# Optimization experiments

Measured on AMD Instinct MI355X. Metric: run time of the kernel, lower is better.

Reference implementation:

```python
import jax, jax.numpy as jnp
import numpy as np

B, T, H, E = 8, 2048, 512, 512

def setup_inputs() -> dict:
    key = jax.random.key(0)
    k1, k2, k3, k4 = jax.random.split(key, 4)
    tokens = jax.random.normal(k1, (B, T, H), dtype=jnp.float32)
    # Linear(hidden,embed,bias=False): stored as (in,out) so Q = tokens @ Wq
    Wq = jax.random.normal(k2, (H, E), dtype=jnp.float32) / np.sqrt(H)
    Wk = jax.random.normal(k3, (H, E), dtype=jnp.float32) / np.sqrt(H)
    Wv = jax.random.normal(k4, (H, H), dtype=jnp.float32) / np.sqrt(H)
    return {"tokens": tokens, "Wq": Wq, "Wk": Wk, "Wv": Wv}

def reference(tokens, Wq, Wk, Wv):
    Q = jnp.einsum('bth,he->bte', tokens, Wq)   # [B,T,E]
    K = jnp.einsum('bsh,he->bse', tokens, Wk)   # [B,T,E]
    V = jnp.einsum('bsh,hd->bsd', tokens, Wv)   # [B,T,H]
    scoremats = jnp.einsum('bte,bse->bts', Q, K)  # [B,T,T]
    # NOTE: softmax over axis=1 (query axis t), matching F.softmax(dim=1)
    attnmats = jax.nn.softmax(scoremats, axis=1)
    ctx_vecs = jnp.einsum('bts,bsh->bth', attnmats, V)  # [B,T,H]
    return ctx_vecs
```

## Files before the change

### kernel.cpp

```cpp
#include <hip/hip_runtime.h>

typedef _Float16 f16;
typedef _Float16 f16x8 __attribute__((ext_vector_type(8)));
typedef _Float16 f16x4 __attribute__((ext_vector_type(4)));
typedef float   f32x4 __attribute__((ext_vector_type(4)));

#define LOG2E 1.44269504088896340736f

__device__ __forceinline__ f32x4 mfma_f16(f16x8 a, f16x8 b, f32x4 c){
  return __builtin_amdgcn_mfma_f32_16x16x32_f16(a, b, c, 0, 0, 0);
}
__device__ __forceinline__ float fexp2(float x){ return __builtin_amdgcn_exp2f(x); }

__device__ __forceinline__ void gld16(void* lds, const void* g){
  __builtin_amdgcn_global_load_lds(
      (const __attribute__((address_space(1))) unsigned int*)g,
      (__attribute__((address_space(3))) unsigned int*)lds,
      16, 0, 0);
}


__global__ __launch_bounds__(256) void k_prep_g(const float* __restrict__ Wq,
                                                const float* __restrict__ Wk,
                                                f16* __restrict__ B16){
  __shared__ float ak[32][36];
  __shared__ float aq[32][36];
  const int n0 = blockIdx.y * 32, e0 = blockIdx.x * 32;
  const int u = threadIdx.x;
  const int ty = u >> 4, tx = u & 15;
  float acc[2][2] = {};
  for (int x0 = 0; x0 < 512; x0 += 32){
    __syncthreads();
    {
      int r = u >> 3, c4 = (u & 7) * 4;
      *(float4*)&ak[r][c4] = *(const float4*)&Wk[(n0 + r) * 512 + x0 + c4];
      *(float4*)&aq[r][c4] = *(const float4*)&Wq[(e0 + r) * 512 + x0 + c4];
    }
    __syncthreads();
#pragma unroll 8
    for (int x = 0; x < 32; ++x){
      float k0 = ak[ty * 2 + 0][x], k1 = ak[ty * 2 + 1][x];
      float q0 = aq[tx * 2 + 0][x], q1 = aq[tx * 2 + 1][x];
      acc[0][0] += k0 * q0; acc[0][1] += k0 * q1;
      acc[1][0] += k1 * q0; acc[1][1] += k1 * q1;
    }
  }
#pragma unroll
  for (int i = 0; i < 2; ++i)
#pragma unroll
    for (int j = 0; j < 2; ++j)
      B16[(size_t)(n0 + ty * 2 + i) * 512 + e0 + tx * 2 + j] = (f16)acc[i][j];
}

__global__ __launch_bounds__(256) void k_prep_wv(const float* __restrict__ Wv,
                                                 f16* __restrict__ B16){
  __shared__ float t[64][72];
  const int e0 = blockIdx.x * 64, h0 = blockIdx.y * 64;
  const int u = threadIdx.x;
#pragma unroll
  for (int k = 0; k < 4; ++k){
    int idx = u + k * 256; int r = idx >> 4, c4 = (idx & 15) * 4;
    *(float4*)&t[r][c4] = *(const float4*)&Wv[(e0 + r) * 512 + h0 + c4];
  }
  __syncthreads();
#pragma unroll
  for (int k = 0; k < 4; ++k){
    int idx = u + k * 256; int j = idx >> 4, i4 = (idx & 15) * 4;
#pragma unroll
    for (int c = 0; c < 4; ++c)
      B16[(size_t)(512 + h0 + j) * 512 + e0 + i4 + c] = (f16)t[i4 + c][j];
  }
}

__global__ __launch_bounds__(256) void k_cast(const float* __restrict__ tok,
                                              f16* __restrict__ T16){
  int i = blockIdx.x * 256 + threadIdx.x;
  const float4* p = (const float4*)tok + (size_t)i * 2;
  float4 a = p[0], b = p[1];
  f16x8 h;
  h[0] = (f16)a.x; h[1] = (f16)a.y; h[2] = (f16)a.z; h[3] = (f16)a.w;
  h[4] = (f16)b.x; h[5] = (f16)b.y; h[6] = (f16)b.z; h[7] = (f16)b.w;
  *((f16x8*)T16 + i) = h;
}

__global__ __launch_bounds__(256, 4) void k_gemm(const f16* __restrict__ T16,
                                                 const f16* __restrict__ B16,
                                                 f16* __restrict__ QG,
                                                 f16* __restrict__ VT){
  __shared__ __align__(16) f16 Abuf[128 * 64];
  __shared__ __align__(16) f16 Bbuf[128 * 64];
  const int tb = blockIdx.x, nb = blockIdx.y;
  const int u = threadIdx.x;
  const int w = u >> 6, l = u & 63, lr = l & 15, lq = l >> 4;
  const int sx8 = (l & 7) ^ (l >> 3), hi8 = l >> 3;
  const int wm = (w & 1) * 64, wn = (w >> 1) * 64;
  f32x4 acc[4][4] = {};
  const f16* sa0 = T16 + (size_t)tb * 128 * 512;
  const f16* sb0 = B16 + (size_t)nb * 128 * 512;
  for (int c = 0; c < 8; ++c){
    {
      const f16* sa = sa0 + c * 64;
      const f16* sb_ = sb0 + c * 64;
#pragma unroll
      for (int k = 0; k < 4; ++k){
        int i = w * 4 + k;
        int row = i * 8 + hi8;
        gld16((char*)Abuf + i * 1024, sa  + (size_t)row * 512 + sx8 * 8);
        gld16((char*)Bbuf + i * 1024, sb_ + (size_t)row * 512 + sx8 * 8);
      }
    }
    __syncthreads();
#pragma unroll
    for (int es = 0; es < 2; ++es){
      f16x8 af[4], bf[4];
#pragma unroll
      for (int mt = 0; mt < 4; ++mt){
        int row = wm + mt * 16 + lr;
        af[mt] = *(const f16x8*)((const char*)Abuf + row * 128 + (((es * 4 + lq) ^ (row & 7)) << 4));
      }
#pragma unroll
      for (int nt = 0; nt < 4; ++nt){
        int row = wn + nt * 16 + lr;
        bf[nt] = *(const f16x8*)((const char*)Bbuf + row * 128 + (((es * 4 + lq) ^ (row & 7)) << 4));
      }
#pragma unroll
      for (int mt = 0; mt < 4; ++mt)
#pragma unroll
        for (int nt = 0; nt < 4; ++nt)
          acc[mt][nt] = mfma_f16(af[mt], bf[nt], acc[mt][nt]);
    }
    __syncthreads();
  }
  if (nb < 4){
#pragma unroll
    for (int mt = 0; mt < 4; ++mt)
#pragma unroll
      for (int nt = 0; nt < 4; ++nt){
        int n = nb * 128 + wn + nt * 16 + lr;
        int r0 = tb * 128 + wm + mt * 16 + lq * 4;
#pragma unroll
        for (int j = 0; j < 4; ++j)
          QG[(size_t)(r0 + j) * 512 + n] = (f16)acc[mt][nt][j];
      }
  } else {
#pragma unroll
    for (int mt = 0; mt < 4; ++mt)
#pragma unroll
      for (int nt = 0; nt < 4; ++nt){
        int h = (nb - 4) * 128 + wn + nt * 16 + lr;
        int r0 = tb * 128 + wm + mt * 16 + lq * 4;
        int bq = r0 >> 11, s = r0 & 2047;
        f16x4 hv;
#pragma unroll
        for (int j = 0; j < 4; ++j) hv[j] = (f16)acc[mt][nt][j];
        *(f16x4*)&VT[(size_t)(bq * 512 + h) * 2048 + s] = hv;
      }
  }
}

__global__ __launch_bounds__(512, 2) void k_pass1p(const f16* __restrict__ T16,
                                                   const f16* __restrict__ QG,
                                                   f16* __restrict__ Pp,
                                                   float* __restrict__ Mp,
                                                   float* __restrict__ Dp){
  const int gid = blockIdx.x;
  const int b = gid & 7;
  const int sb = (gid >> 3) & 15;
  const int tb = gid >> 7;
  const int u = threadIdx.x;
  const int w = u >> 6, l = u & 63, lr = l & 15, lq = l >> 4;
  const int sx8 = (l & 7) ^ (l >> 3), hi8 = l >> 3;
  const int ws2 = w & 1, wt2 = w >> 1;
  const int wm = ws2 * 64, wn = wt2 * 64;

  __shared__ __align__(16) f16 Abuf[128 * 64];
  __shared__ __align__(16) f16 Bbuf[256 * 64];
  __shared__ float redM[4][128];
  __shared__ float redD[4][128];

  f32x4 acc[4][4] = {};
  const f16* sa0 = T16 + ((size_t)(b * 2048 + sb * 128) * 512);
  const f16* sb0 = QG + ((size_t)(b * 2048 + tb * 256) * 512);
  for (int c = 0; c < 8; ++c){
    {
      const f16* sa = sa0 + c * 64;
      const f16* sb_ = sb0 + c * 64;
#pragma unroll
      for (int k = 0; k < 2; ++k){
        int i = w * 2 + k;
        int row = i * 8 + hi8;
        gld16((char*)Abuf + i * 1024, sa + (size_t)row * 512 + sx8 * 8);
      }
#pragma unroll
      for (int k = 0; k < 4; ++k){
        int i = w * 4 + k;
        int row = i * 8 + hi8;
        gld16((char*)Bbuf + i * 1024, sb_ + (size_t)row * 512 + sx8 * 8);
      }
    }
    __syncthreads();
#pragma unroll
    for (int es = 0; es < 2; ++es){
      f16x8 af[4], bf[4];
#pragma unroll
      for (int mt = 0; mt < 4; ++mt){
        int row = wm + mt * 16 + lr;
        af[mt] = *(const f16x8*)((const char*)Abuf + row * 128 + (((es * 4 + lq) ^ (row & 7)) << 4));
      }
#pragma unroll
      for (int nt = 0; nt < 4; ++nt){
        int row = wn + nt * 16 + lr;
        bf[nt] = *(const f16x8*)((const char*)Bbuf + row * 128 + (((es * 4 + lq) ^ (row & 7)) << 4));
      }
#pragma unroll
      for (int mt = 0; mt < 4; ++mt)
#pragma unroll
        for (int nt = 0; nt < 4; ++nt)
          acc[mt][nt] = mfma_f16(af[mt], bf[nt], acc[mt][nt]);
    }
    __syncthreads();
  }
#pragma unroll
  for (int mt = 0; mt < 4; ++mt)
#pragma unroll
    for (int nt = 0; nt < 4; ++nt)
#pragma unroll
      for (int j = 0; j < 4; ++j)
        acc[mt][nt][j] *= LOG2E;
#pragma unroll
  for (int mt = 0; mt < 4; ++mt)
#pragma unroll
    for (int j = 0; j < 4; ++j){
      float m2 = fmaxf(fmaxf(acc[mt][0][j], acc[mt][1][j]),
                       fmaxf(acc[mt][2][j], acc[mt][3][j]));
#pragma unroll
      for (int off = 1; off <= 8; off <<= 1)
        m2 = fmaxf(m2, __shfl_xor(m2, off, 64));
      if (lr == 0) redM[wt2][wm + mt * 16 + lq * 4 + j] = m2;
    }
  __syncthreads();
  float M[4][4];
#pragma unroll
  for (int mt = 0; mt < 4; ++mt)
#pragma unroll
    for (int j = 0; j < 4; ++j){
      int idx = wm + mt * 16 + lq * 4 + j;
      M[mt][j] = fmaxf(fmaxf(redM[0][idx], redM[1][idx]),
                       fmaxf(redM[2][idx], redM[3][idx]));
    }
#pragma unroll
  for (int mt = 0; mt < 4; ++mt)
#pragma unroll
    for (int nt = 0; nt < 4; ++nt){
      int t = tb * 256 + wn + nt * 16 + lr;
      f16x4 h4;
#pragma unroll
      for (int j = 0; j < 4; ++j){
        float p = fexp2(acc[mt][nt][j] - M[mt][j]);
        acc[mt][nt][j] = p;
        h4[j] = (f16)p;
      }
      *(f16x4*)&Pp[(size_t)(b * 2048 + t) * 2048 + sb * 128 + wm + mt * 16 + lq * 4] = h4;
    }
#pragma unroll
  for (int mt = 0; mt < 4; ++mt)
#pragma unroll
    for (int j = 0; j < 4; ++j){
      float sd = acc[mt][0][j] + acc[mt][1][j] + acc[mt][2][j] + acc[mt][3][j];
#pragma unroll
      for (int off = 1; off <= 8; off <<= 1)
        sd += __shfl_xor(sd, off, 64);
      if (lr == 0) redD[wt2][wm + mt * 16 + lq * 4 + j] = sd;
    }
  __syncthreads();
  if (u < 128){
    int sg = b * 2048 + sb * 128 + u;
    Mp[tb * 16384 + sg] = fmaxf(fmaxf(redM[0][u], redM[1][u]),
                                fmaxf(redM[2][u], redM[3][u]));
    Dp[tb * 16384 + sg] = redD[0][u] + redD[1][u] + redD[2][u] + redD[3][u];
  }
}

__global__ __launch_bounds__(256) void k_scm(const float* __restrict__ Mp,
                                             const float* __restrict__ Dp,
                                             f16* __restrict__ SC16){
  int i = blockIdx.x * 256 + threadIdx.x;
  float mv[8];
  float m = -1e30f;
#pragma unroll
  for (int ti = 0; ti < 8; ++ti){
    mv[ti] = Mp[ti * 16384 + i];
    m = fmaxf(m, mv[ti]);
  }
  float d = 0.f;
#pragma unroll
  for (int ti = 0; ti < 8; ++ti)
    d += Dp[ti * 16384 + i] * fexp2(mv[ti] - m);
  float rd = 1.0f / d;
#pragma unroll
  for (int ti = 0; ti < 8; ++ti)
    SC16[ti * 16384 + i] = (f16)(fexp2(mv[ti] - m) * rd);
}

__global__ __launch_bounds__(256, 2) void k_pass2p(const f16* __restrict__ Pp,
                                                   const f16* __restrict__ VT,
                                                   const f16* __restrict__ SC16,
                                                   float* __restrict__ out){
  const int gid = blockIdx.x;
  const int b = gid & 7;
  const int tb = (gid >> 3) & 15;
  const int hb = gid >> 7;
  const int ti = tb >> 1;
  const int u = threadIdx.x;
  const int w = u >> 6, l = u & 63, lr = l & 15, lq = l >> 4;
  const int sx8 = (l & 7) ^ (l >> 3), hi8 = l >> 3;
  const int wm = (w & 1) * 64, wn = (w >> 1) * 64;

  __shared__ __align__(16) f16 Abuf[2][128 * 64];
  __shared__ __align__(16) f16 Bbuf[2][128 * 64];
  __shared__ __align__(16) f16 scl[2048];

  {
    f16x8 v = *(const f16x8*)&SC16[(size_t)ti * 16384 + b * 2048 + u * 8];
    *(f16x8*)&scl[u * 8] = v;
  }
  f32x4 acc[4][4] = {};
  auto stage = [&](int c, int buf){
    const f16* sa = VT + ((size_t)(b * 512 + hb * 128) * 2048 + c * 64);
    const f16* sb_ = Pp + ((size_t)(b * 2048 + tb * 128) * 2048 + c * 64);
#pragma unroll
    for (int k = 0; k < 4; ++k){
      int i = w * 4 + k;
      int row = i * 8 + hi8;
      gld16((char*)&Abuf[buf][0] + i * 1024, sa  + (size_t)row * 2048 + sx8 * 8);
      gld16((char*)&Bbuf[buf][0] + i * 1024, sb_ + (size_t)row * 2048 + sx8 * 8);
    }
  };
  stage(0, 0);
  for (int c = 0; c < 32; ++c){
    __syncthreads();
    if (c < 31) stage(c + 1, (c + 1) & 1);
    const f16* A = &Abuf[c & 1][0];
    const f16* B = &Bbuf[c & 1][0];
#pragma unroll
    for (int es = 0; es < 2; ++es){
      f16x8 sclv = *(const f16x8*)&scl[c * 64 + es * 32 + lq * 8];
      f16x8 af[4], bf[4];
#pragma unroll
      for (int mt = 0; mt < 4; ++mt){
        int row = wm + mt * 16 + lr;
        af[mt] = *(const f16x8*)((const char*)A + row * 128 + (((es * 4 + lq) ^ (row & 7)) << 4));
      }
#pragma unroll
      for (int nt = 0; nt < 4; ++nt){
        int row = wn + nt * 16 + lr;
        f16x8 p = *(const f16x8*)((const char*)B + row * 128 + (((es * 4 + lq) ^ (row & 7)) << 4));
        bf[nt] = p * sclv;
      }
#pragma unroll
      for (int mt = 0; mt < 4; ++mt)
#pragma unroll
        for (int nt = 0; nt < 4; ++nt)
          acc[mt][nt] = mfma_f16(af[mt], bf[nt], acc[mt][nt]);
    }
  }
#pragma unroll
  for (int mt = 0; mt < 4; ++mt)
#pragma unroll
    for (int nt = 0; nt < 4; ++nt){
      int t = tb * 128 + wn + nt * 16 + lr;
      int h = hb * 128 + wm + mt * 16 + lq * 4;
      float4 v;
      v.x = acc[mt][nt][0]; v.y = acc[mt][nt][1];
      v.z = acc[mt][nt][2]; v.w = acc[mt][nt][3];
      *(float4*)&out[(size_t)(b * 2048 + t) * 512 + h] = v;
    }
}

extern "C" void kernel_launch(void* const* d_in, const int* in_sizes, int n_in,
                              void* d_out, int out_size, void* d_ws, size_t ws_size,
                              hipStream_t stream){
  (void)in_sizes; (void)n_in; (void)out_size; (void)ws_size;
  const float* tokens = (const float*)d_in[0];
  const float* Wq = (const float*)d_in[1];
  const float* Wk = (const float*)d_in[2];
  const float* Wv = (const float*)d_in[3];
  char* ws = (char*)d_ws;
  f16*    T16 = (f16*)(ws);
  f16*    QG  = (f16*)(ws + (16u << 20));
  f16*    VT  = (f16*)(ws + (32u << 20));
  f16*    B16 = (f16*)(ws + (48u << 20));
  f16*    SC16= (f16*)(ws + (50u << 20));
  float*  Mp  = (float*)(ws + (51u << 20));
  float*  Dp  = (float*)(ws + (52u << 20));
  f16*    Pp  = (f16*)(ws + (54u << 20));
  float* out = (float*)d_out;

  k_prep_g <<<dim3(16, 16), dim3(256), 0, stream>>>(Wq, Wk, B16);
  k_prep_wv<<<dim3(8, 8),   dim3(256), 0, stream>>>(Wv, B16);
  k_cast   <<<dim3(4096),   dim3(256), 0, stream>>>(tokens, T16);
  k_gemm   <<<dim3(128, 8), dim3(256), 0, stream>>>(T16, B16, QG, VT);
  k_pass1p <<<dim3(1024),   dim3(512), 0, stream>>>(T16, QG, Pp, Mp, Dp);
  k_scm    <<<dim3(64),     dim3(256), 0, stream>>>(Mp, Dp, SC16);
  k_pass2p <<<dim3(512),    dim3(256), 0, stream>>>(Pp, VT, SC16, out);
}
```

Baseline: 161.2 us.

## Shrink pass2 tile to 64x128, drop double buffering, double grid

The P·V pass now gives each block a 64-wide slice of H instead of 128 and drops LDS double buffering for a single buffer guarded by two barriers. The grid doubles to 1024 blocks and launch bounds ask for 4 blocks per CU, with fewer accumulators per thread. The aim is higher occupancy and more blocks to spread across CUs, so latency is hidden by other waves rather than by prefetch. In exchange, the P tile is reloaded from global memory twice as often and loads no longer overlap compute inside a block.

```diff
diff --git a/kernel.cpp b/kernel.cpp
--- a/kernel.cpp
+++ b/kernel.cpp
@@ -302,7 +302,7 @@
     SC16[ti * 16384 + i] = (f16)(fexp2(mv[ti] - m) * rd);
 }
 
-__global__ __launch_bounds__(256, 2) void k_pass2p(const f16* __restrict__ Pp,
+__global__ __launch_bounds__(256, 4) void k_pass2p(const f16* __restrict__ Pp,
                                                    const f16* __restrict__ VT,
                                                    const f16* __restrict__ SC16,
                                                    float* __restrict__ out){
@@ -314,65 +314,68 @@
   const int u = threadIdx.x;
   const int w = u >> 6, l = u & 63, lr = l & 15, lq = l >> 4;
   const int sx8 = (l & 7) ^ (l >> 3), hi8 = l >> 3;
-  const int wm = (w & 1) * 64, wn = (w >> 1) * 64;
-
-  __shared__ __align__(16) f16 Abuf[2][128 * 64];
-  __shared__ __align__(16) f16 Bbuf[2][128 * 64];
+
+  __shared__ __align__(16) f16 Abuf[64 * 64];
+  __shared__ __align__(16) f16 Bbuf[128 * 64];
   __shared__ __align__(16) f16 scl[2048];
 
   {
     f16x8 v = *(const f16x8*)&SC16[(size_t)ti * 16384 + b * 2048 + u * 8];
     *(f16x8*)&scl[u * 8] = v;
   }
-  f32x4 acc[4][4] = {};
-  auto stage = [&](int c, int buf){
-    const f16* sa = VT + ((size_t)(b * 512 + hb * 128) * 2048 + c * 64);
-    const f16* sb_ = Pp + ((size_t)(b * 2048 + tb * 128) * 2048 + c * 64);
-#pragma unroll
-    for (int k = 0; k < 4; ++k){
-      int i = w * 4 + k;
-      int row = i * 8 + hi8;
-      gld16((char*)&Abuf[buf][0] + i * 1024, sa  + (size_t)row * 2048 + sx8 * 8);
-      gld16((char*)&Bbuf[buf][0] + i * 1024, sb_ + (size_t)row * 2048 + sx8 * 8);
-    }
-  };
-  stage(0, 0);
+  f32x4 acc[4][2] = {};
+  const f16* sa0 = VT + ((size_t)(b * 512 + hb * 64) * 2048);
+  const f16* sb0 = Pp + ((size_t)(b * 2048 + tb * 128) * 2048);
   for (int c = 0; c < 32; ++c){
-    __syncthreads();
-    if (c < 31) stage(c + 1, (c + 1) & 1);
-    const f16* A = &Abuf[c & 1][0];
-    const f16* B = &Bbuf[c & 1][0];
+    {
+      const f16* sa = sa0 + c * 64;
+      const f16* sb_ = sb0 + c * 64;
+#pragma unroll
+      for (int k = 0; k < 2; ++k){
+        int i = w * 2 + k;
+        int row = i * 8 + hi8;
+        gld16((char*)Abuf + i * 1024, sa + (size_t)row * 2048 + sx8 * 8);
+      }
+#pragma unroll
+      for (int k = 0; k < 4; ++k){
+        int i = w * 4 + k;
+        int row = i * 8 + hi8;
+        gld16((char*)Bbuf + i * 1024, sb_ + (size_t)row * 2048 + sx8 * 8);
+      }
+    }
+    __syncthreads();
 #pragma unroll
     for (int es = 0; es < 2; ++es){
       f16x8 sclv = *(const f16x8*)&scl[c * 64 + es * 32 + lq * 8];
-      f16x8 af[4], bf[4];
-#pragma unroll
-      for (int mt = 0; mt < 4; ++mt){
-        int row = wm + mt * 16 + lr;
-        af[mt] = *(const f16x8*)((const char*)A + row * 128 + (((es * 4 + lq) ^ (row & 7)) << 4));
-      }
-#pragma unroll
-      for (int nt = 0; nt < 4; ++nt){
-        int row = wn + nt * 16 + lr;
-        f16x8 p = *(const f16x8*)((const char*)B + row * 128 + (((es * 4 + lq) ^ (row & 7)) << 4));
+      f16x8 af[4], bf[2];
+#pragma unroll
+      for (int ht = 0; ht < 4; ++ht){
+        int row = ht * 16 + lr;
+        af[ht] = *(const f16x8*)((const char*)Abuf + row * 128 + (((es * 4 + lq) ^ (row & 7)) << 4));
+      }
+#pragma unroll
+      for (int nt = 0; nt < 2; ++nt){
+        int row = w * 32 + nt * 16 + lr;
+        f16x8 p = *(const f16x8*)((const char*)Bbuf + row * 128 + (((es * 4 + lq) ^ (row & 7)) << 4));
         bf[nt] = p * sclv;
       }
 #pragma unroll
-      for (int mt = 0; mt < 4; ++mt)
-#pragma unroll
-        for (int nt = 0; nt < 4; ++nt)
-          acc[mt][nt] = mfma_f16(af[mt], bf[nt], acc[mt][nt]);
-    }
-  }
-#pragma unroll
-  for (int mt = 0; mt < 4; ++mt)
-#pragma unroll
-    for (int nt = 0; nt < 4; ++nt){
-      int t = tb * 128 + wn + nt * 16 + lr;
-      int h = hb * 128 + wm + mt * 16 + lq * 4;
+      for (int ht = 0; ht < 4; ++ht)
+#pragma unroll
+        for (int nt = 0; nt < 2; ++nt)
+          acc[ht][nt] = mfma_f16(af[ht], bf[nt], acc[ht][nt]);
+    }
+    __syncthreads();
+  }
+#pragma unroll
+  for (int ht = 0; ht < 4; ++ht)
+#pragma unroll
+    for (int nt = 0; nt < 2; ++nt){
+      int t = tb * 128 + w * 32 + nt * 16 + lr;
+      int h = hb * 64 + ht * 16 + lq * 4;
       float4 v;
-      v.x = acc[mt][nt][0]; v.y = acc[mt][nt][1];
-      v.z = acc[mt][nt][2]; v.w = acc[mt][nt][3];
+      v.x = acc[ht][nt][0]; v.y = acc[ht][nt][1];
+      v.z = acc[ht][nt][2]; v.w = acc[ht][nt][3];
       *(float4*)&out[(size_t)(b * 2048 + t) * 512 + h] = v;
     }
 }
@@ -402,5 +405,5 @@
   k_gemm   <<<dim3(128, 8), dim3(256), 0, stream>>>(T16, B16, QG, VT);
   k_pass1p <<<dim3(1024),   dim3(512), 0, stream>>>(T16, QG, Pp, Mp, Dp);
   k_scm    <<<dim3(64),     dim3(256), 0, stream>>>(Mp, Dp, SC16);
-  k_pass2p <<<dim3(512),    dim3(256), 0, stream>>>(Pp, VT, SC16, out);
-}
+  k_pass2p <<<dim3(1024),   dim3(256), 0, stream>>>(Pp, VT, SC16, out);
+}
```

New measurement: 162.1 us. About the same (+0.5%).
